# Kernel tuning notes

Measured on AMD Instinct MI355X. Metric: run time of the kernel, lower is better.

The kernel has to match this reference:

```python
import math
import jax, jax.numpy as jnp
import numpy as np

N, E, D, B, S, H = 16384, 196608, 256, 256, 64, 8
DH = D // H
BN_INV = 1.0 / math.sqrt(1.0 + 1e-5)  # eval-mode BN: mean=0, var=1, eps=1e-5
LOG2 = math.log(2.0)


def _mlp(x, w1, b1, w2, b2):
    # Linear -> SiLU -> Linear
    return jax.nn.silu(x @ w1 + b1) @ w2 + b2


def _bn(x, g, b):
    # BatchNorm1d in eval mode with running_mean=0, running_var=1
    return x * (BN_INV * g) + b


def _graph_ln(x, g, b):
    # pyg LayerNorm(mode='graph') called with batch=None: normalize over all nodes+features
    mu = jnp.mean(x)
    xc = x - mu
    var = jnp.mean(xc * xc)
    return xc * jax.lax.rsqrt(var + 1e-5) * g + b


def _forward(x, edge_index, edge_attr,
             node_w1, node_b1, node_w2, node_b2,
             c_w1, c_b1, c_w2, c_b2,
             bn_e_g, bn_e_b, bn_h_g, bn_h_b,
             n1l_g, n1l_b, n1a_g, n1a_b, n2_g, n2_b,
             wq, bq, wk, bk, wv, bv, wo, bo,
             aff_w1, aff_b1, aff_w2, aff_b2,
             fn_g, fn_b, fc_w1, fc_b1, fc_w2, fc_b2):
    row, col = edge_index[0], edge_index[1]

    # ---- PotNetConvGate local branch ----
    # A, B, V, U MLPs (all take node features) computed with stacked weights [4,D,D]
    hid = jax.nn.silu(jnp.einsum('nd,kdf->knf', x, node_w1) + node_b1[:, None, :])
    node_out = jnp.einsum('knf,kfg->kng', hid, node_w2) + node_b2[:, None, :]
    h_A, h_B, h_V, h_U = node_out[0], node_out[1], node_out[2], node_out[3]
    e_C = _mlp(edge_attr, c_w1, c_b1, c_w2, c_b2)  # [E,D]

    score = jax.nn.relu(_bn(h_A[row] + h_B[col] + e_C, bn_e_g, bn_e_b))  # [E,D]
    e_new = edge_attr + score

    # pyg softmax over edges grouped by destination node (col), per channel
    m = jax.ops.segment_max(e_new, col, num_segments=N)        # [N,D]
    ex = jnp.exp(e_new - m[col])
    s = jax.ops.segment_sum(ex, col, num_segments=N)           # [N,D]
    gated = ex / (s[col] + 1e-16)

    msg = gated * (h_V[col] + e_new)
    aggr = jax.ops.segment_sum(msg, col, num_segments=N)       # [N,D]
    h_local = jax.nn.silu(x + _bn(h_U + aggr, bn_h_g, bn_h_b))
    # e_out = silu(e_new + edge_attr)  # edge output, not used downstream for node output
    h_local = _bn(h_local, n1l_g, n1l_b)  # norm1_local

    # ---- global Transformer branch (equal-size graphs -> dense reshape, full mask) ----
    hd = x.reshape(B, S, D)
    q = (hd @ wq + bq).reshape(B, S, H, DH).transpose(0, 2, 1, 3)
    k = (hd @ wk + bk).reshape(B, S, H, DH).transpose(0, 2, 1, 3)
    v = (hd @ wv + bv).reshape(B, S, H, DH).transpose(0, 2, 1, 3)
    att = jax.nn.softmax(jnp.einsum('bhqd,bhkd->bhqk', q, k) / math.sqrt(DH), axis=-1)
    o = jnp.einsum('bhqk,bhkd->bhqd', att, v).transpose(0, 2, 1, 3).reshape(B, S, D)
    h_attn = (o @ wo + bo).reshape(N, D)

    h_attn = _bn(h_attn + x, n1a_g, n1a_b)  # norm1_attn
    t = jax.nn.gelu(h_attn @ aff_w1 + aff_b1, approximate=False) @ aff_w2 + aff_b2
    h_attn = _graph_ln(t + x, fn_g, fn_b)   # feed_norm

    # ---- fuse branches (mean over stacked outputs) ----
    h_new = (h_local + h_attn) * 0.5

    # ---- _ff_block: fc = Linear -> ShiftedSoftplus -> Linear ----
    ssp = jax.nn.softplus(h_new @ fc_w1 + fc_b1) - LOG2
    out = ssp @ fc_w2 + fc_b2
    return _bn(out + h_new, n2_g, n2_b)  # norm2


def setup_inputs():
    key = jax.random.key(0)
    ks = iter(jax.random.split(key, 64))
    sc = 1.0 / math.sqrt(D)
    def w(shape):
        return jax.random.normal(next(ks), shape, jnp.float32) * sc
    z = lambda *s: jnp.zeros(s, jnp.float32)
    o = lambda *s: jnp.ones(s, jnp.float32)
    return {
        'x': jax.random.normal(next(ks), (N, D), jnp.float32),
        'edge_index': jax.random.randint(next(ks), (2, E), 0, N, jnp.int32),
        'edge_attr': jax.random.normal(next(ks), (E, D), jnp.float32),
        'node_w1': w((4, D, D)), 'node_b1': z(4, D),
        'node_w2': w((4, D, D)), 'node_b2': z(4, D),
        'c_w1': w((D, D)), 'c_b1': z(D), 'c_w2': w((D, D)), 'c_b2': z(D),
        'bn_e_g': o(D), 'bn_e_b': z(D), 'bn_h_g': o(D), 'bn_h_b': z(D),
        'n1l_g': o(D), 'n1l_b': z(D), 'n1a_g': o(D), 'n1a_b': z(D),
        'n2_g': o(D), 'n2_b': z(D),
        'wq': w((D, D)), 'bq': z(D), 'wk': w((D, D)), 'bk': z(D),
        'wv': w((D, D)), 'bv': z(D), 'wo': w((D, D)), 'bo': z(D),
        'aff_w1': w((D, 2 * D)), 'aff_b1': z(2 * D),
        'aff_w2': w((2 * D, D)), 'aff_b2': z(D),
        'fn_g': o(D), 'fn_b': z(D),
        'fc_w1': w((D, 2 * D)), 'fc_b1': z(2 * D),
        'fc_w2': w((2 * D, D)), 'fc_b2': z(D),
    }


def reference(x, edge_index, edge_attr,
              node_w1, node_b1, node_w2, node_b2,
              c_w1, c_b1, c_w2, c_b2,
              bn_e_g, bn_e_b, bn_h_g, bn_h_b,
              n1l_g, n1l_b, n1a_g, n1a_b, n2_g, n2_b,
              wq, bq, wk, bk, wv, bv, wo, bo,
              aff_w1, aff_b1, aff_w2, aff_b2,
              fn_g, fn_b, fc_w1, fc_b1, fc_w2, fc_b2):
    return _forward(x, edge_index, edge_attr,
                    node_w1, node_b1, node_w2, node_b2,
                    c_w1, c_b1, c_w2, c_b2,
                    bn_e_g, bn_e_b, bn_h_g, bn_h_b,
                    n1l_g, n1l_b, n1a_g, n1a_b, n2_g, n2_b,
                    wq, bq, wk, bk, wv, bv, wo, bo,
                    aff_w1, aff_b1, aff_w2, aff_b2,
                    fn_g, fn_b, fc_w1, fc_b1, fc_w2, fc_b2)
```

## Files before the change

kernel.cpp:

```cpp
#include <hip/hip_runtime.h>
#include <hip/hip_bf16.h>
#include <stdint.h>

#define NN 16384
#define NE 196608
#define DD 256
#define ND 4194304
#define BNINV 0.9999950000374997f
#define LOG2F_ 0.6931471805599453f

typedef __attribute__((ext_vector_type(8))) short short8v;
typedef __attribute__((ext_vector_type(4))) float float4v;

__device__ __forceinline__ float b2f(__hip_bfloat16 v) { return __bfloat162float(v); }
__device__ __forceinline__ __hip_bfloat16 f2b(float v) { return __float2bfloat16(v); }

__device__ __forceinline__ void gl_lds16(const __hip_bfloat16* g, __hip_bfloat16* l) {
  __builtin_amdgcn_global_load_lds((const __attribute__((address_space(1))) void*)g,
                                   (__attribute__((address_space(3))) void*)l, 16, 0, 0);
}

__device__ __forceinline__ float rdf(const void* p, size_t i, int fl) {
  return fl ? b2f(((const __hip_bfloat16*)p)[i]) : ((const float*)p)[i];
}

__device__ __forceinline__ short8v cvt8(float4v f0, float4v f1) {
  short8v s;
#pragma unroll
  for (int i = 0; i < 4; ++i) {
    __hip_bfloat16 h0 = f2b(f0[i]), h1 = f2b(f1[i]);
    s[i] = *(short*)&h0;
    s[4 + i] = *(short*)&h1;
  }
  return s;
}

__device__ __forceinline__ void stage_w(const __hip_bfloat16* W, __hip_bfloat16* buf,
                                        int kb, int tid) {
#pragma unroll
  for (int r = 0; r < 4; ++r) {
    const int c2 = r * 256 + tid;
    gl_lds16(W + (c2 >> 2) * 256 + kb * 32 + (c2 & 3) * 8, buf + c2 * 8);
  }
}

#define OFF_WT    0ul
#define OFF_PB    2883584ul
#define OFF_XB    2899968ul
#define OFF_HN    11288576ul
#define OFF_HL    44843008ul
#define OFF_EN    162283520ul
#define OFF_QKV   262946816ul
#define OFF_O     313278464ul
#define OFF_HATTN 321667072ul
#define OFF_HIDN  330055680ul
#define OFF_U     346832896ul
#define OFF_HNEW  363610112ul
#define OFF_HNEWB 380387328ul
#define OFF_TAIL  388775936ul

#define PB_NB1   0
#define PB_NB2   1024
#define PB_CB1   2048
#define PB_CB2   2304
#define PB_QKVB  2560
#define PB_BO    3328
#define PB_AB1   3584
#define PB_AB2   4096
#define PB_FB1   4352
#define PB_FB2   4864
#define PB_BNEG  5120
#define PB_BNEB  5376
#define PB_BNHG  5632
#define PB_BNHB  5888
#define PB_N1LG  6144
#define PB_N1LB  6400
#define PB_N1AG  6656
#define PB_N1AB  6912
#define PB_N2G   7168
#define PB_N2B   7424
#define PB_FNG   7680
#define PB_FNB   7936

__global__ void probe_kernel(const uint32_t* bneg_raw, int* flag) {
  if (threadIdx.x == 0 && blockIdx.x == 0)
    *flag = (bneg_raw[0] == 0x3F803F80u) ? 1 : 0;
}

struct PJobs {
  const void* src[24];
  int off[24];
  int len[24];
};

__global__ void canon_params(PJobs jb, __hip_bfloat16* PB, const int* flagp) {
  const int fl = *flagp;
  const int j = blockIdx.x;
  const void* src = jb.src[j];
  const int off = jb.off[j], len = jb.len[j];
  for (int i = threadIdx.x; i < len; i += 256) PB[off + i] = f2b(rdf(src, i, fl));
}

__global__ void canon_x(const void* x, __hip_bfloat16* XB, const int* flagp) {
  const int fl = *flagp;
  const size_t i = (size_t)blockIdx.x * 256 + threadIdx.x;
  XB[i] = f2b(rdf(x, i, fl));
}

struct TJobsF {
  const void* src[18];
  __hip_bfloat16* dst[18];
  int R[18];
  int C[18];
  int RB[18];
};

__global__ void transpose_rb(TJobsF jb, const int* flagp) {
  __shared__ __hip_bfloat16 tile[32][33];
  const int fl = *flagp;
  const int j = blockIdx.z;
  const int R = jb.R[j], C = jb.C[j], RB = jb.RB[j];
  const int c0 = blockIdx.x * 32, r0 = blockIdx.y * 32;
  if (c0 >= C || r0 >= R) return;
  const void* src = jb.src[j];
  __hip_bfloat16* dst = jb.dst[j];
  const int tx = threadIdx.x, ty = threadIdx.y;
#pragma unroll
  for (int i = 0; i < 4; ++i)
    tile[ty + i * 8][tx] = f2b(rdf(src, (size_t)(RB + r0 + ty + i * 8) * C + c0 + tx, fl));
  __syncthreads();
#pragma unroll
  for (int i = 0; i < 4; ++i)
    dst[(long)(c0 + ty + i * 8) * R + r0 + tx] = tile[tx][ty + i * 8];
}

__global__ void prep_kernel(int* counts, double* stats) {
  const int i = blockIdx.x * blockDim.x + threadIdx.x;
  if (i < NN) counts[i] = 0;
  if (i == 0) counts[NN] = 0;
  if (i < 2) stats[i] = 0.0;
}

template <int ACT, int RES, int BNM, int OUTBF, int DUALOUT>
__global__ __launch_bounds__(256) void gemm_bt(
    const void* __restrict__ Avp, const __hip_bfloat16* __restrict__ Wt,
    const __hip_bfloat16* __restrict__ bias, const void* __restrict__ Res,
    const __hip_bfloat16* __restrict__ bng, const __hip_bfloat16* __restrict__ bnb,
    void* __restrict__ Cout, const int* __restrict__ flagp,
    int M, int N, int K, long boff, long az, long wz, long bz, long cz) {
  __shared__ __align__(16) __hip_bfloat16 sA[2][128 * 32];
  __shared__ __align__(16) __hip_bfloat16 sB[2][128 * 32];
  const int fl = DUALOUT ? *flagp : 1;
  const int z = blockIdx.z;
  const long aoff = boff + (long)z * az;
  const __hip_bfloat16* Ab = (const __hip_bfloat16*)Avp + aoff;
  Wt += (long)z * wz;
  bias += (long)z * bz;
  const long coff = (long)z * cz;
  const int tid = threadIdx.x;
  const int lane = tid & 63;
  const int wid = tid >> 6;
  const int wm = wid >> 1, wn = wid & 1;
  const int l16 = lane & 15, lq = lane >> 4;
  const long am0 = (long)blockIdx.y * 128;
  const long bn0 = (long)blockIdx.x * 128;

  float4v acc[4][4] = {};

  const int nK = K >> 5;
#pragma unroll
  for (int r = 0; r < 2; ++r) {
    const int c = tid + r * 256;
    gl_lds16(Ab + (am0 + (c >> 2)) * K + (c & 3) * 8, sA[0] + c * 8);
    gl_lds16(Wt + (bn0 + (c >> 2)) * K + (c & 3) * 8, sB[0] + c * 8);
  }
  __syncthreads();

  for (int kb = 0; kb < nK; ++kb) {
    const int cur = kb & 1;
    if (kb + 1 < nK) {
      const int nx = cur ^ 1;
#pragma unroll
      for (int r = 0; r < 2; ++r) {
        const int c = tid + r * 256;
        gl_lds16(Ab + (am0 + (c >> 2)) * K + (kb + 1) * 32 + (c & 3) * 8, sA[nx] + c * 8);
        gl_lds16(Wt + (bn0 + (c >> 2)) * K + (kb + 1) * 32 + (c & 3) * 8, sB[nx] + c * 8);
      }
    }
    const short* pA = (const short*)sA[cur];
    const short* pB = (const short*)sB[cur];
    short8v af[4], bv_[4];
#pragma unroll
    for (int mi = 0; mi < 4; ++mi)
      af[mi] = *(const short8v*)(pA + (wm * 64 + mi * 16 + l16) * 32 + lq * 8);
#pragma unroll
    for (int ni = 0; ni < 4; ++ni)
      bv_[ni] = *(const short8v*)(pB + (wn * 64 + ni * 16 + l16) * 32 + lq * 8);
#pragma unroll
    for (int mi = 0; mi < 4; ++mi)
#pragma unroll
      for (int ni = 0; ni < 4; ++ni)
        acc[mi][ni] =
            __builtin_amdgcn_mfma_f32_16x16x32_bf16(af[mi], bv_[ni], acc[mi][ni], 0, 0, 0);
    if (kb + 1 < nK) __syncthreads();
  }

  const __hip_bfloat16* Rb = (const __hip_bfloat16*)Res;
  const float* Rf = (const float*)Res;
#pragma unroll
  for (int mi = 0; mi < 4; ++mi) {
#pragma unroll
    for (int ni = 0; ni < 4; ++ni) {
#pragma unroll
      for (int r = 0; r < 4; ++r) {
        const long row = am0 + wm * 64 + mi * 16 + lq * 4 + r;
        const long col = bn0 + wn * 64 + ni * 16 + l16;
        float v = acc[mi][ni][r] + b2f(bias[col]);
        if (ACT == 1) v = v / (1.f + __expf(-v));
        else if (ACT == 2) v = 0.5f * v * (1.f + erff(v * 0.7071067811865476f));
        else if (ACT == 3) v = (v > 15.f ? v : log1pf(__expf(v))) - LOG2F_;
        if (RES == 1) v += b2f(Rb[row * N + col]);
        else if (RES == 2) v += Rf[row * N + col];
        if (BNM) v = v * (BNINV * b2f(bng[col])) + b2f(bnb[col]);
        if (DUALOUT) {
          if (fl) ((__hip_bfloat16*)Cout)[coff + row * N + col] = f2b(v);
          else ((float*)Cout)[coff + row * N + col] = v;
        } else if (OUTBF) {
          ((__hip_bfloat16*)Cout)[coff + row * N + col] = f2b(v);
        } else {
          ((float*)Cout)[coff + row * N + col] = v;
        }
      }
    }
  }
}

template <int EPI, int ASRC>
__global__ __launch_bounds__(256) void mlp_fused(
    const void* __restrict__ Avp, const __hip_bfloat16* __restrict__ W1t,
    const __hip_bfloat16* __restrict__ b1, const __hip_bfloat16* __restrict__ W2t,
    const __hip_bfloat16* __restrict__ b2, __hip_bfloat16* __restrict__ Out,
    const int* __restrict__ ei, const void* __restrict__ eattr,
    const __hip_bfloat16* __restrict__ HA, __hip_bfloat16* __restrict__ EN,
    const __hip_bfloat16* __restrict__ PB, const int* __restrict__ perm,
    const int* __restrict__ flagp, long wz, long cz) {
  __shared__ __align__(16) __hip_bfloat16 sW[2][256 * 32];
  __shared__ __align__(16) __hip_bfloat16 sH[64 * 264];
  const int fl = (ASRC == 1) ? *flagp : 1;
  const int z = blockIdx.z;
  W1t += (long)z * wz;
  W2t += (long)z * wz;
  b1 += z * 256;
  b2 += z * 256;
  const int tid = threadIdx.x;
  const int lane = tid & 63;
  const int wn = tid >> 6;
  const int l16 = lane & 15, lq = lane >> 4;
  const long m0 = (long)blockIdx.y * 64;
  const __hip_bfloat16* Ab = (const __hip_bfloat16*)Avp;
  const float* Af = (const float*)Avp;
  const int arow = tid >> 2, ako = (tid & 3) * 8;

  float4v acc[4][4] = {};

  if (ASRC == 1 && fl == 0) {
    const float* ap = Af + (m0 + arow) * 256 + ako;
    ((short8v*)sH)[tid] = cvt8(*(const float4v*)ap, *(const float4v*)(ap + 4));
  } else {
    gl_lds16(Ab + (m0 + arow) * 256 + ako, sH + tid * 8);
  }
  stage_w(W1t, sW[0], 0, tid);
  __syncthreads();

  for (int kb = 0; kb < 8; ++kb) {
    const int cur = kb & 1;
    float4v pf0, pf1;
    int pend = 0;
    if (kb < 7) {
      if (ASRC == 1 && fl == 0) {
        const float* ap = Af + (m0 + arow) * 256 + (kb + 1) * 32 + ako;
        pf0 = *(const float4v*)ap;
        pf1 = *(const float4v*)(ap + 4);
        pend = 1;
      } else {
        gl_lds16(Ab + (m0 + arow) * 256 + (kb + 1) * 32 + ako,
                 sH + (cur ^ 1) * 2048 + tid * 8);
      }
      stage_w(W1t, sW[cur ^ 1], kb + 1, tid);
    }
    const short* pA = (const short*)(sH + cur * 2048);
    const short* pW = (const short*)sW[cur];
    short8v af[4], bf_[4];
#pragma unroll
    for (int mi = 0; mi < 4; ++mi)
      af[mi] = *(const short8v*)(pA + (mi * 16 + l16) * 32 + lq * 8);
#pragma unroll
    for (int ni = 0; ni < 4; ++ni)
      bf_[ni] = *(const short8v*)(pW + (wn * 64 + ni * 16 + l16) * 32 + lq * 8);
#pragma unroll
    for (int mi = 0; mi < 4; ++mi)
#pragma unroll
      for (int ni = 0; ni < 4; ++ni)
        acc[mi][ni] =
            __builtin_amdgcn_mfma_f32_16x16x32_bf16(af[mi], bf_[ni], acc[mi][ni], 0, 0, 0);
    if (pend) ((short8v*)(sH + (cur ^ 1) * 2048))[tid] = cvt8(pf0, pf1);
    __syncthreads();
  }

  {
    short* hp = (short*)sH;
#pragma unroll
    for (int mi = 0; mi < 4; ++mi)
#pragma unroll
      for (int ni = 0; ni < 4; ++ni)
#pragma unroll
        for (int r = 0; r < 4; ++r) {
          const int row = mi * 16 + lq * 4 + r;
          const int col = wn * 64 + ni * 16 + l16;
          float v = acc[mi][ni][r] + b2f(b1[col]);
          v = v / (1.f + __expf(-v));
          __hip_bfloat16 hb = f2b(v);
          hp[row * 264 + col] = *(short*)&hb;
          acc[mi][ni][r] = 0.f;
        }
  }
  stage_w(W2t, sW[0], 0, tid);
  __syncthreads();

  for (int kb = 0; kb < 8; ++kb) {
    const int cur = kb & 1;
    if (kb < 7) stage_w(W2t, sW[cur ^ 1], kb + 1, tid);
    const short* pW = (const short*)sW[cur];
    short8v af[4], bf_[4];
#pragma unroll
    for (int mi = 0; mi < 4; ++mi)
      af[mi] = *(const short8v*)((const short*)sH + (mi * 16 + l16) * 264 + kb * 32 + lq * 8);
#pragma unroll
    for (int ni = 0; ni < 4; ++ni)
      bf_[ni] = *(const short8v*)(pW + (wn * 64 + ni * 16 + l16) * 32 + lq * 8);
#pragma unroll
    for (int mi = 0; mi < 4; ++mi)
#pragma unroll
      for (int ni = 0; ni < 4; ++ni)
        acc[mi][ni] =
            __builtin_amdgcn_mfma_f32_16x16x32_bf16(af[mi], bf_[ni], acc[mi][ni], 0, 0, 0);
    if (kb < 7) __syncthreads();
  }

  if (EPI == 0) {
#pragma unroll
    for (int mi = 0; mi < 4; ++mi)
#pragma unroll
      for (int ni = 0; ni < 4; ++ni)
#pragma unroll
        for (int r = 0; r < 4; ++r) {
          const long row = m0 + mi * 16 + lq * 4 + r;
          const int col = wn * 64 + ni * 16 + l16;
          Out[(long)z * cz + row * 256 + col] = f2b(acc[mi][ni][r] + b2f(b2[col]));
        }
  } else {
    const __hip_bfloat16* HB = HA + (size_t)ND;
#pragma unroll
    for (int mi = 0; mi < 4; ++mi)
#pragma unroll
      for (int r = 0; r < 4; ++r) {
        const long ge = m0 + mi * 16 + lq * 4 + r;
        const int rr = ei[ge];
        const int cc = ei[NE + ge];
        const long pe = perm[ge];
#pragma unroll
        for (int ni = 0; ni < 4; ++ni) {
          const int col = wn * 64 + ni * 16 + l16;
          float v = acc[mi][ni][r] + b2f(b2[col]);
          v += b2f(HA[(size_t)rr * DD + col]) + b2f(HB[(size_t)cc * DD + col]);
          v = v * (BNINV * b2f(PB[PB_BNEG + col])) + b2f(PB[PB_BNEB + col]);
          v = fmaxf(v, 0.f);
          v += rdf(eattr, (size_t)ge * DD + col, fl);
          EN[(size_t)pe * DD + col] = f2b(v);
        }
      }
  }
}

__global__ void count_kernel(const int* __restrict__ ei, int* __restrict__ counts) {
  const int e = blockIdx.x * 256 + threadIdx.x;
  if (e < NE) atomicAdd(&counts[ei[NE + e]], 1);
}

__global__ __launch_bounds__(1024) void scan_kernel(int* __restrict__ counts,
                                                    int* __restrict__ cursor) {
  __shared__ int part[1024];
  const int t = threadIdx.x;
  const int base = t * 16;
  int ss = 0;
#pragma unroll
  for (int i = 0; i < 16; ++i) ss += counts[base + i];
  part[t] = ss;
  __syncthreads();
  for (int off = 1; off < 1024; off <<= 1) {
    int v = (t >= off) ? part[t - off] : 0;
    __syncthreads();
    part[t] += v;
    __syncthreads();
  }
  int run = part[t] - ss;
  for (int i = 0; i < 16; ++i) {
    const int cv = counts[base + i];
    counts[base + i] = run;
    cursor[base + i] = run;
    run += cv;
  }
  if (t == 1023) counts[NN] = run;
}

__global__ void scatter_kernel(const int* __restrict__ ei, int* __restrict__ cursor,
                               int* __restrict__ perm) {
  const int e = blockIdx.x * 256 + threadIdx.x;
  if (e < NE) {
    const int p = atomicAdd(&cursor[ei[NE + e]], 1);
    perm[e] = p;
  }
}

__global__ __launch_bounds__(256) void segment_kernel(
    const int* __restrict__ offs, const __hip_bfloat16* __restrict__ EN,
    const __hip_bfloat16* __restrict__ hV, const __hip_bfloat16* __restrict__ hU,
    const __hip_bfloat16* __restrict__ XB, const __hip_bfloat16* __restrict__ PB,
    float* __restrict__ hlocal) {
  const int n = blockIdx.x;
  const int d = threadIdx.x;
  const int beg = offs[n], end = offs[n + 1];
  float sa = 0.f, sb = 0.f;
  int p = beg;
  for (; p + 4 <= end; p += 4) {
    const float v0 = b2f(EN[(size_t)(p + 0) * DD + d]);
    const float v1 = b2f(EN[(size_t)(p + 1) * DD + d]);
    const float v2 = b2f(EN[(size_t)(p + 2) * DD + d]);
    const float v3 = b2f(EN[(size_t)(p + 3) * DD + d]);
    const float e0 = __expf(v0), e1 = __expf(v1), e2 = __expf(v2), e3 = __expf(v3);
    sa += (e0 + e1) + (e2 + e3);
    sb += (e0 * v0 + e1 * v1) + (e2 * v2 + e3 * v3);
  }
  for (; p < end; ++p) {
    const float v = b2f(EN[(size_t)p * DD + d]);
    const float e = __expf(v);
    sa += e;
    sb += e * v;
  }
  const float hv = b2f(hV[(size_t)n * DD + d]);
  const float ag = (hv * sa + sb) / (sa + 1e-16f);
  const float t1 =
      (b2f(hU[(size_t)n * DD + d]) + ag) * (BNINV * b2f(PB[PB_BNHG + d])) + b2f(PB[PB_BNHB + d]);
  float s1 = b2f(XB[(size_t)n * DD + d]) + t1;
  s1 = s1 / (1.f + __expf(-s1));
  s1 = s1 * (BNINV * b2f(PB[PB_N1LG + d])) + b2f(PB[PB_N1LB + d]);
  hlocal[(size_t)n * DD + d] = s1;
}

__global__ __launch_bounds__(256) void attn_kernel(const float* __restrict__ QKV,
                                                   __hip_bfloat16* __restrict__ O) {
  __shared__ float sq[64][33], sk[64][33], sv[64][33];
  __shared__ float sp[64][65];
  const int bh = blockIdx.x;
  const int b = bh >> 3, h = bh & 7;
  const int tid = threadIdx.x;
  const float* Q = QKV;
  const float* Kp = QKV + (size_t)ND;
  const float* Vp = QKV + 2 * (size_t)ND;
#pragma unroll
  for (int j = 0; j < 8; ++j) {
    const int idx = j * 256 + tid;
    const int s = idx >> 5, dh = idx & 31;
    const size_t ga = ((size_t)(b * 64 + s)) * DD + h * 32 + dh;
    sq[s][dh] = Q[ga];
    sk[s][dh] = Kp[ga];
    sv[s][dh] = Vp[ga];
  }
  __syncthreads();
  const int row = tid >> 2, l4 = tid & 3;
  float qr[32];
#pragma unroll
  for (int d = 0; d < 32; ++d) qr[d] = sq[row][d];
  float sc[16];
  float mx = -1e30f;
#pragma unroll
  for (int jj = 0; jj < 16; ++jj) {
    const int j = l4 * 16 + jj;
    float dot = 0.f;
#pragma unroll
    for (int d = 0; d < 32; ++d) dot += qr[d] * sk[j][d];
    dot *= 0.17677669529663687f;
    sc[jj] = dot;
    mx = fmaxf(mx, dot);
  }
  mx = fmaxf(mx, __shfl_xor(mx, 1));
  mx = fmaxf(mx, __shfl_xor(mx, 2));
  float se = 0.f;
#pragma unroll
  for (int jj = 0; jj < 16; ++jj) {
    sc[jj] = __expf(sc[jj] - mx);
    se += sc[jj];
  }
  se += __shfl_xor(se, 1);
  se += __shfl_xor(se, 2);
  const float inv = 1.f / se;
#pragma unroll
  for (int jj = 0; jj < 16; ++jj) sp[row][l4 * 16 + jj] = sc[jj] * inv;
  __syncthreads();
#pragma unroll
  for (int k8 = 0; k8 < 8; ++k8) {
    const int dh = l4 * 8 + k8;
    float acc = 0.f;
#pragma unroll
    for (int j = 0; j < 64; ++j) acc += sp[row][j] * sv[j][dh];
    O[((size_t)(b * 64 + row)) * DD + h * 32 + dh] = f2b(acc);
  }
}

__global__ __launch_bounds__(256) void stats_kernel(const float* __restrict__ U,
                                                    double* __restrict__ st) {
  double s = 0.0, s2 = 0.0;
  for (size_t i = (size_t)blockIdx.x * 256 + threadIdx.x; i < (size_t)ND;
       i += (size_t)gridDim.x * 256) {
    const double v = (double)U[i];
    s += v;
    s2 += v * v;
  }
  for (int o = 32; o > 0; o >>= 1) {
    s += __shfl_down(s, o);
    s2 += __shfl_down(s2, o);
  }
  __shared__ double wred[4][2];
  const int lane = threadIdx.x & 63, w = threadIdx.x >> 6;
  if (lane == 0) {
    wred[w][0] = s;
    wred[w][1] = s2;
  }
  __syncthreads();
  if (threadIdx.x == 0) {
    double a = 0, bb = 0;
    for (int i = 0; i < 4; ++i) {
      a += wred[i][0];
      bb += wred[i][1];
    }
    atomicAdd(&st[0], a);
    atomicAdd(&st[1], bb);
  }
}

__global__ void finalize_stats(double* st) {
  if (threadIdx.x == 0 && blockIdx.x == 0) {
    const double mu = st[0] / (double)ND;
    const double var = st[1] / (double)ND - mu * mu;
    float* f = (float*)(st + 2);
    f[0] = (float)mu;
    f[1] = (float)(1.0 / sqrt(var + 1e-5));
  }
}

__global__ void hnew_kernel(const float* __restrict__ U, const float* __restrict__ hlocal,
                            const double* __restrict__ st, const __hip_bfloat16* __restrict__ PB,
                            float* __restrict__ HNEW, __hip_bfloat16* __restrict__ HNEWB) {
  const size_t i = (size_t)blockIdx.x * 256 + threadIdx.x;
  const float* f = (const float*)(st + 2);
  const float mu = f[0], rs = f[1];
  const int d = (int)(i & 255);
  const float ha = (U[i] - mu) * rs * b2f(PB[PB_FNG + d]) + b2f(PB[PB_FNB + d]);
  const float hn = 0.5f * (hlocal[i] + ha);
  HNEW[i] = hn;
  HNEWB[i] = f2b(hn);
}

extern "C" void kernel_launch(void* const* d_in, const int* in_sizes, int n_in, void* d_out,
                              int out_size, void* d_ws, size_t ws_size, hipStream_t stream) {
  (void)in_sizes; (void)n_in; (void)out_size; (void)ws_size;
  const void* x = d_in[0];
  const int* ei = (const int*)d_in[1];
  const void* eattr = d_in[2];

  uint8_t* ws = (uint8_t*)d_ws;
  __hip_bfloat16* WT = (__hip_bfloat16*)(ws + OFF_WT);
  __hip_bfloat16* PB = (__hip_bfloat16*)(ws + OFF_PB);
  __hip_bfloat16* XB = (__hip_bfloat16*)(ws + OFF_XB);
  __hip_bfloat16* HN = (__hip_bfloat16*)(ws + OFF_HN);
  float* HL = (float*)(ws + OFF_HL);
  __hip_bfloat16* EN = (__hip_bfloat16*)(ws + OFF_EN);
  float* QKV = (float*)(ws + OFF_QKV);
  __hip_bfloat16* O = (__hip_bfloat16*)(ws + OFF_O);
  __hip_bfloat16* HATTN = (__hip_bfloat16*)(ws + OFF_HATTN);
  __hip_bfloat16* HIDN = (__hip_bfloat16*)(ws + OFF_HIDN);
  float* U = (float*)(ws + OFF_U);
  float* HNEW = (float*)(ws + OFF_HNEW);
  __hip_bfloat16* HNEWB = (__hip_bfloat16*)(ws + OFF_HNEWB);
  uint8_t* tail = ws + OFF_TAIL;
  int* counts = (int*)tail;
  int* cursor = (int*)(tail + 66048ul);
  int* perm = (int*)(tail + 132096ul);
  double* stats = (double*)(tail + 918528ul);
  int* flag = (int*)(tail + 918592ul);

  probe_kernel<<<1, 64, 0, stream>>>((const uint32_t*)d_in[11], flag);

  PJobs pj;
  {
    const int srcidx[24] = {4, 6, 8, 10, 22, 24, 26, 28, 30, 32, 36, 38,
                            11, 12, 13, 14, 15, 16, 17, 18, 19, 20, 33, 34};
    const int dstoff[24] = {PB_NB1, PB_NB2, PB_CB1, PB_CB2, PB_QKVB, PB_QKVB + 256,
                            PB_QKVB + 512, PB_BO, PB_AB1, PB_AB2, PB_FB1, PB_FB2,
                            PB_BNEG, PB_BNEB, PB_BNHG, PB_BNHB, PB_N1LG, PB_N1LB,
                            PB_N1AG, PB_N1AB, PB_N2G, PB_N2B, PB_FNG, PB_FNB};
    const int lens[24] = {1024, 1024, 256, 256, 256, 256, 256, 256, 512, 256, 512, 256,
                          256, 256, 256, 256, 256, 256, 256, 256, 256, 256, 256, 256};
    for (int i = 0; i < 24; ++i) {
      pj.src[i] = d_in[srcidx[i]];
      pj.off[i] = dstoff[i];
      pj.len[i] = lens[i];
    }
  }
  canon_params<<<24, 256, 0, stream>>>(pj, PB, flag);
  canon_x<<<NN, 256, 0, stream>>>(x, XB, flag);

  TJobsF jf;
  for (int j = 0; j < 4; ++j) {
    jf.src[j] = d_in[3]; jf.dst[j] = WT + j * 65536;
    jf.R[j] = 256; jf.C[j] = 256; jf.RB[j] = j * 256;
    jf.src[4 + j] = d_in[5]; jf.dst[4 + j] = WT + 262144 + j * 65536;
    jf.R[4 + j] = 256; jf.C[4 + j] = 256; jf.RB[4 + j] = j * 256;
  }
  {
    const int widx[10] = {7, 9, 21, 23, 25, 27, 29, 31, 35, 37};
    const long wdst[10] = {524288, 589824, 655360, 720896, 786432, 851968,
                           917504, 1048576, 1179648, 1310720};
    const int wR[10] = {256, 256, 256, 256, 256, 256, 256, 512, 256, 512};
    const int wC[10] = {256, 256, 256, 256, 256, 256, 512, 256, 512, 256};
    for (int j = 0; j < 10; ++j) {
      jf.src[8 + j] = d_in[widx[j]]; jf.dst[8 + j] = WT + wdst[j];
      jf.R[8 + j] = wR[j]; jf.C[8 + j] = wC[j]; jf.RB[8 + j] = 0;
    }
  }
  transpose_rb<<<dim3(16, 16, 18), dim3(32, 8), 0, stream>>>(jf, flag);

  prep_kernel<<<64, 256, 0, stream>>>(counts, stats);

  count_kernel<<<768, 256, 0, stream>>>(ei, counts);
  scan_kernel<<<1, 1024, 0, stream>>>(counts, cursor);
  scatter_kernel<<<768, 256, 0, stream>>>(ei, cursor, perm);

  mlp_fused<0, 0><<<dim3(1, 256, 4), 256, 0, stream>>>(
      XB, WT, PB + PB_NB1, WT + 262144, PB + PB_NB2, HN,
      nullptr, nullptr, nullptr, nullptr, nullptr, nullptr, flag, 65536, ND);

  mlp_fused<1, 1><<<dim3(1, 3072, 1), 256, 0, stream>>>(
      eattr, WT + 524288, PB + PB_CB1, WT + 589824, PB + PB_CB2, nullptr,
      ei, eattr, HN, EN, PB, perm, flag, 0, 0);

  segment_kernel<<<NN, 256, 0, stream>>>(counts, EN, HN + 2 * (size_t)ND,
                                         HN + 3 * (size_t)ND, XB, PB, HL);

  gemm_bt<0, 0, 0, 0, 0><<<dim3(2, 128, 3), 256, 0, stream>>>(
      XB, WT + 655360, PB + PB_QKVB, nullptr, nullptr, nullptr, QKV, flag,
      NN, DD, DD, 0, 0, 65536, 256, ND);
  attn_kernel<<<2048, 256, 0, stream>>>(QKV, O);
  gemm_bt<0, 1, 1, 1, 0><<<dim3(2, 128, 1), 256, 0, stream>>>(
      O, WT + 851968, PB + PB_BO, XB, PB + PB_N1AG, PB + PB_N1AB, HATTN, flag,
      NN, DD, DD, 0, 0, 0, 0, 0);

  gemm_bt<2, 0, 0, 1, 0><<<dim3(4, 128, 1), 256, 0, stream>>>(
      HATTN, WT + 917504, PB + PB_AB1, nullptr, nullptr, nullptr, HIDN, flag,
      NN, 512, DD, 0, 0, 0, 0, 0);
  gemm_bt<0, 1, 0, 0, 0><<<dim3(2, 128, 1), 256, 0, stream>>>(
      HIDN, WT + 1048576, PB + PB_AB2, XB, nullptr, nullptr, U, flag,
      NN, DD, 512, 0, 0, 0, 0, 0);

  stats_kernel<<<1024, 256, 0, stream>>>(U, stats);
  finalize_stats<<<1, 64, 0, stream>>>(stats);
  hnew_kernel<<<NN, 256, 0, stream>>>(U, HL, stats, PB, HNEW, HNEWB);

  gemm_bt<3, 0, 0, 1, 0><<<dim3(4, 128, 1), 256, 0, stream>>>(
      HNEWB, WT + 1179648, PB + PB_FB1, nullptr, nullptr, nullptr, HIDN, flag,
      NN, 512, DD, 0, 0, 0, 0, 0);
  gemm_bt<0, 2, 1, 1, 1><<<dim3(2, 128, 1), 256, 0, stream>>>(
      HIDN, WT + 1310720, PB + PB_FB2, HNEW, PB + PB_N2G, PB + PB_N2B, d_out, flag,
      NN, DD, 512, 0, 0, 0, 0, 0);
}
```

Baseline: 938.4 us.

## Deepen GEMM LDS prefetch with explicit waitcnt and pre-convert edge attrs to bf16

Both the generic GEMM and the fused MLP kernels now prefetch two K-tiles ahead. They replace __syncthreads with explicit vmcnt/lgkmcnt waits and raw barriers, so global-to-LDS loads overlap with MFMA work for longer. A new canon_e kernel converts fp32 edge attributes to bf16 up front, letting the edge MLP always use the async global_load_lds path and a dedicated A buffer instead of in-register conversion. The cost is an extra full pass over the edge attribute tensor plus more workspace, and the hand-placed waitcnt counts must match the number of issued loads.

Result: faster. 888.7 us (-5.3%).

```diff
diff --git a/kernel.cpp b/kernel.cpp
--- a/kernel.cpp
+++ b/kernel.cpp
@@ -20,6 +20,13 @@
                                    (__attribute__((address_space(3))) void*)l, 16, 0, 0);
 }
 
+#define VMW5 asm volatile("s_waitcnt vmcnt(5)" ::: "memory")
+#define VMW4 asm volatile("s_waitcnt vmcnt(4)" ::: "memory")
+#define VMW0 asm volatile("s_waitcnt vmcnt(0)" ::: "memory")
+#define LKW0 asm volatile("s_waitcnt lgkmcnt(0)" ::: "memory")
+#define SB __builtin_amdgcn_s_barrier()
+#define SCB __builtin_amdgcn_sched_barrier(0)
+
 __device__ __forceinline__ float rdf(const void* p, size_t i, int fl) {
   return fl ? b2f(((const __hip_bfloat16*)p)[i]) : ((const float*)p)[i];
 }
@@ -33,15 +40,6 @@
     s[4 + i] = *(short*)&h1;
   }
   return s;
-}
-
-__device__ __forceinline__ void stage_w(const __hip_bfloat16* W, __hip_bfloat16* buf,
-                                        int kb, int tid) {
-#pragma unroll
-  for (int r = 0; r < 4; ++r) {
-    const int c2 = r * 256 + tid;
-    gl_lds16(W + (c2 >> 2) * 256 + kb * 32 + (c2 & 3) * 8, buf + c2 * 8);
-  }
 }
 
 #define OFF_WT    0ul
@@ -58,6 +56,7 @@
 #define OFF_HNEW  363610112ul
 #define OFF_HNEWB 380387328ul
 #define OFF_TAIL  388775936ul
+#define OFF_EB    390070272ul
 
 #define PB_NB1   0
 #define PB_NB2   1024
@@ -85,6 +84,15 @@
 __global__ void probe_kernel(const uint32_t* bneg_raw, int* flag) {
   if (threadIdx.x == 0 && blockIdx.x == 0)
     *flag = (bneg_raw[0] == 0x3F803F80u) ? 1 : 0;
+}
+
+__global__ void canon_e(const float* __restrict__ e, __hip_bfloat16* __restrict__ EB,
+                        const int* __restrict__ flagp) {
+  if (*flagp) return;
+  const size_t i = ((size_t)blockIdx.x * 256 + threadIdx.x) * 8;
+  const float4v f0 = *(const float4v*)(e + i);
+  const float4v f1 = *(const float4v*)(e + i + 4);
+  *(short8v*)((short*)EB + i) = cvt8(f0, f1);
 }
 
 struct PJobs {
@@ -168,25 +176,22 @@
   float4v acc[4][4] = {};
 
   const int nK = K >> 5;
-#pragma unroll
-  for (int r = 0; r < 2; ++r) {
-    const int c = tid + r * 256;
-    gl_lds16(Ab + (am0 + (c >> 2)) * K + (c & 3) * 8, sA[0] + c * 8);
-    gl_lds16(Wt + (bn0 + (c >> 2)) * K + (c & 3) * 8, sB[0] + c * 8);
-  }
-  __syncthreads();
+  auto STG = [&](int t, int b) {
+#pragma unroll
+    for (int r = 0; r < 2; ++r) {
+      const int c = tid + r * 256;
+      gl_lds16(Ab + (am0 + (c >> 2)) * (long)K + (long)t * 32 + (c & 3) * 8, sA[b] + c * 8);
+      gl_lds16(Wt + (bn0 + (c >> 2)) * (long)K + (long)t * 32 + (c & 3) * 8, sB[b] + c * 8);
+    }
+  };
+
+  STG(0, 0);
+  STG(1, 1);
+  VMW4;
+  SB;
 
   for (int kb = 0; kb < nK; ++kb) {
     const int cur = kb & 1;
-    if (kb + 1 < nK) {
-      const int nx = cur ^ 1;
-#pragma unroll
-      for (int r = 0; r < 2; ++r) {
-        const int c = tid + r * 256;
-        gl_lds16(Ab + (am0 + (c >> 2)) * K + (kb + 1) * 32 + (c & 3) * 8, sA[nx] + c * 8);
-        gl_lds16(Wt + (bn0 + (c >> 2)) * K + (kb + 1) * 32 + (c & 3) * 8, sB[nx] + c * 8);
-      }
-    }
     const short* pA = (const short*)sA[cur];
     const short* pB = (const short*)sB[cur];
     short8v af[4], bv_[4];
@@ -196,13 +201,20 @@
 #pragma unroll
     for (int ni = 0; ni < 4; ++ni)
       bv_[ni] = *(const short8v*)(pB + (wn * 64 + ni * 16 + l16) * 32 + lq * 8);
+    LKW0;
+    SCB;
+    SB;
+    if (kb + 2 < nK) STG(kb + 2, cur);
 #pragma unroll
     for (int mi = 0; mi < 4; ++mi)
 #pragma unroll
       for (int ni = 0; ni < 4; ++ni)
         acc[mi][ni] =
             __builtin_amdgcn_mfma_f32_16x16x32_bf16(af[mi], bv_[ni], acc[mi][ni], 0, 0, 0);
-    if (kb + 1 < nK) __syncthreads();
+    if (kb + 1 < nK) {
+      if (kb + 2 < nK) VMW4; else VMW0;
+      SB;
+    }
   }
 
   const __hip_bfloat16* Rb = (const __hip_bfloat16*)Res;
@@ -235,19 +247,21 @@
   }
 }
 
-template <int EPI, int ASRC>
+template <int EPI>
 __global__ __launch_bounds__(256) void mlp_fused(
-    const void* __restrict__ Avp, const __hip_bfloat16* __restrict__ W1t,
+    const __hip_bfloat16* __restrict__ Adef, const __hip_bfloat16* __restrict__ W1t,
     const __hip_bfloat16* __restrict__ b1, const __hip_bfloat16* __restrict__ W2t,
     const __hip_bfloat16* __restrict__ b2, __hip_bfloat16* __restrict__ Out,
     const int* __restrict__ ei, const void* __restrict__ eattr,
-    const __hip_bfloat16* __restrict__ HA, __hip_bfloat16* __restrict__ EN,
-    const __hip_bfloat16* __restrict__ PB, const int* __restrict__ perm,
-    const int* __restrict__ flagp, long wz, long cz) {
+    const __hip_bfloat16* __restrict__ EB, const __hip_bfloat16* __restrict__ HA,
+    __hip_bfloat16* __restrict__ EN, const __hip_bfloat16* __restrict__ PB,
+    const int* __restrict__ perm, const int* __restrict__ flagp, long wz, long cz) {
+  __shared__ __align__(16) __hip_bfloat16 sA[2][64 * 32];
   __shared__ __align__(16) __hip_bfloat16 sW[2][256 * 32];
   __shared__ __align__(16) __hip_bfloat16 sH[64 * 264];
-  const int fl = (ASRC == 1) ? *flagp : 1;
   const int z = blockIdx.z;
+  const __hip_bfloat16* Ab =
+      (EPI == 1) ? ((*flagp) ? (const __hip_bfloat16*)eattr : EB) : Adef;
   W1t += (long)z * wz;
   W2t += (long)z * wz;
   b1 += z * 256;
@@ -257,38 +271,27 @@
   const int wn = tid >> 6;
   const int l16 = lane & 15, lq = lane >> 4;
   const long m0 = (long)blockIdx.y * 64;
-  const __hip_bfloat16* Ab = (const __hip_bfloat16*)Avp;
-  const float* Af = (const float*)Avp;
-  const int arow = tid >> 2, ako = (tid & 3) * 8;
+
+  auto STA = [&](int t, int b) {
+    gl_lds16(Ab + (m0 + (tid >> 2)) * 256 + t * 32 + (tid & 3) * 8, sA[b] + tid * 8);
+  };
+  auto STW = [&](const __hip_bfloat16* W, int t, int b) {
+#pragma unroll
+    for (int r = 0; r < 4; ++r) {
+      const int c = r * 256 + tid;
+      gl_lds16(W + (c >> 2) * 256 + t * 32 + (c & 3) * 8, sW[b] + c * 8);
+    }
+  };
 
   float4v acc[4][4] = {};
 
-  if (ASRC == 1 && fl == 0) {
-    const float* ap = Af + (m0 + arow) * 256 + ako;
-    ((short8v*)sH)[tid] = cvt8(*(const float4v*)ap, *(const float4v*)(ap + 4));
-  } else {
-    gl_lds16(Ab + (m0 + arow) * 256 + ako, sH + tid * 8);
-  }
-  stage_w(W1t, sW[0], 0, tid);
-  __syncthreads();
-
+  STA(0, 0); STW(W1t, 0, 0);
+  STA(1, 1); STW(W1t, 1, 1);
+  VMW5;
+  SB;
   for (int kb = 0; kb < 8; ++kb) {
     const int cur = kb & 1;
-    float4v pf0, pf1;
-    int pend = 0;
-    if (kb < 7) {
-      if (ASRC == 1 && fl == 0) {
-        const float* ap = Af + (m0 + arow) * 256 + (kb + 1) * 32 + ako;
-        pf0 = *(const float4v*)ap;
-        pf1 = *(const float4v*)(ap + 4);
-        pend = 1;
-      } else {
-        gl_lds16(Ab + (m0 + arow) * 256 + (kb + 1) * 32 + ako,
-                 sH + (cur ^ 1) * 2048 + tid * 8);
-      }
-      stage_w(W1t, sW[cur ^ 1], kb + 1, tid);
-    }
-    const short* pA = (const short*)(sH + cur * 2048);
+    const short* pA = (const short*)sA[cur];
     const short* pW = (const short*)sW[cur];
     short8v af[4], bf_[4];
 #pragma unroll
@@ -297,14 +300,20 @@
 #pragma unroll
     for (int ni = 0; ni < 4; ++ni)
       bf_[ni] = *(const short8v*)(pW + (wn * 64 + ni * 16 + l16) * 32 + lq * 8);
+    LKW0;
+    SCB;
+    SB;
+    if (kb + 2 < 8) { STA(kb + 2, cur); STW(W1t, kb + 2, cur); }
 #pragma unroll
     for (int mi = 0; mi < 4; ++mi)
 #pragma unroll
       for (int ni = 0; ni < 4; ++ni)
         acc[mi][ni] =
             __builtin_amdgcn_mfma_f32_16x16x32_bf16(af[mi], bf_[ni], acc[mi][ni], 0, 0, 0);
-    if (pend) ((short8v*)(sH + (cur ^ 1) * 2048))[tid] = cvt8(pf0, pf1);
-    __syncthreads();
+    if (kb + 1 < 8) {
+      if (kb + 2 < 8) VMW5; else VMW0;
+      SB;
+    }
   }
 
   {
@@ -324,12 +333,14 @@
           acc[mi][ni][r] = 0.f;
         }
   }
-  stage_w(W2t, sW[0], 0, tid);
-  __syncthreads();
+  STW(W2t, 0, 0);
+  STW(W2t, 1, 1);
+  LKW0;
+  VMW4;
+  SB;
 
   for (int kb = 0; kb < 8; ++kb) {
     const int cur = kb & 1;
-    if (kb < 7) stage_w(W2t, sW[cur ^ 1], kb + 1, tid);
     const short* pW = (const short*)sW[cur];
     short8v af[4], bf_[4];
 #pragma unroll
@@ -338,13 +349,20 @@
 #pragma unroll
     for (int ni = 0; ni < 4; ++ni)
       bf_[ni] = *(const short8v*)(pW + (wn * 64 + ni * 16 + l16) * 32 + lq * 8);
+    LKW0;
+    SCB;
+    SB;
+    if (kb + 2 < 8) STW(W2t, kb + 2, cur);
 #pragma unroll
     for (int mi = 0; mi < 4; ++mi)
 #pragma unroll
       for (int ni = 0; ni < 4; ++ni)
         acc[mi][ni] =
             __builtin_amdgcn_mfma_f32_16x16x32_bf16(af[mi], bf_[ni], acc[mi][ni], 0, 0, 0);
-    if (kb < 7) __syncthreads();
+    if (kb + 1 < 8) {
+      if (kb + 2 < 8) VMW4; else VMW0;
+      SB;
+    }
   }
 
   if (EPI == 0) {
@@ -375,7 +393,7 @@
           v += b2f(HA[(size_t)rr * DD + col]) + b2f(HB[(size_t)cc * DD + col]);
           v = v * (BNINV * b2f(PB[PB_BNEG + col])) + b2f(PB[PB_BNEB + col]);
           v = fmaxf(v, 0.f);
-          v += rdf(eattr, (size_t)ge * DD + col, fl);
+          v += b2f(Ab[(size_t)ge * DD + col]);
           EN[(size_t)pe * DD + col] = f2b(v);
         }
       }
@@ -592,6 +610,7 @@
   float* U = (float*)(ws + OFF_U);
   float* HNEW = (float*)(ws + OFF_HNEW);
   __hip_bfloat16* HNEWB = (__hip_bfloat16*)(ws + OFF_HNEWB);
+  __hip_bfloat16* EBp = (__hip_bfloat16*)(ws + OFF_EB);
   uint8_t* tail = ws + OFF_TAIL;
   int* counts = (int*)tail;
   int* cursor = (int*)(tail + 66048ul);
@@ -600,6 +619,8 @@
   int* flag = (int*)(tail + 918592ul);
 
   probe_kernel<<<1, 64, 0, stream>>>((const uint32_t*)d_in[11], flag);
+
+  canon_e<<<24576, 256, 0, stream>>>((const float*)eattr, EBp, flag);
 
   PJobs pj;
   {
@@ -646,13 +667,13 @@
   scan_kernel<<<1, 1024, 0, stream>>>(counts, cursor);
   scatter_kernel<<<768, 256, 0, stream>>>(ei, cursor, perm);
 
-  mlp_fused<0, 0><<<dim3(1, 256, 4), 256, 0, stream>>>(
+  mlp_fused<0><<<dim3(1, 256, 4), 256, 0, stream>>>(
       XB, WT, PB + PB_NB1, WT + 262144, PB + PB_NB2, HN,
-      nullptr, nullptr, nullptr, nullptr, nullptr, nullptr, flag, 65536, ND);
-
-  mlp_fused<1, 1><<<dim3(1, 3072, 1), 256, 0, stream>>>(
-      eattr, WT + 524288, PB + PB_CB1, WT + 589824, PB + PB_CB2, nullptr,
-      ei, eattr, HN, EN, PB, perm, flag, 0, 0);
+      nullptr, nullptr, nullptr, nullptr, nullptr, PB, nullptr, flag, 65536, ND);
+
+  mlp_fused<1><<<dim3(1, 3072, 1), 256, 0, stream>>>(
+      nullptr, WT + 524288, PB + PB_CB1, WT + 589824, PB + PB_CB2, nullptr,
+      ei, eattr, EBp, HN, EN, PB, perm, flag, 0, 0);
 
   segment_kernel<<<NN, 256, 0, stream>>>(counts, EN, HN + 2 * (size_t)ND,
                                          HN + 3 * (size_t)ND, XB, PB, HL);
```
